# Kernel optimization log

Hardware: AMD Instinct MI355X
Metric: run time of the kernel (lower is better)

Reference implementation:

```python
import jax, jax.numpy as jnp
import numpy as np

M = 24      # number of DeepGravity sub-models
D_IN = 495  # input feature dim
H = 64      # hidden dim
L = 5       # hidden layers per sub-model


def setup_inputs() -> dict:
    key = jax.random.key(0)
    ks = jax.random.split(key, 7)
    s = 1.0 / np.sqrt(D_IN)
    sh = 1.0 / np.sqrt(H)
    return {
        "x": jax.random.normal(ks[0], (65536, D_IN), dtype=jnp.float32),
        "W_in": jax.random.uniform(ks[1], (M, D_IN, H), jnp.float32, -s, s),
        "b_in": jax.random.uniform(ks[2], (M, H), jnp.float32, -s, s),
        "W_h": jax.random.uniform(ks[3], (M, L, H, H), jnp.float32, -sh, sh),
        "b_h": jax.random.uniform(ks[4], (M, L, H), jnp.float32, -sh, sh),
        "W_out": jax.random.uniform(ks[5], (M, H), jnp.float32, -sh, sh),
        "b_out": jax.random.uniform(ks[6], (M,), jnp.float32, -sh, sh),
    }


def reference(x, W_in, b_in, W_h, b_h, W_out, b_out):
    # Batched input projection across all 24 models: [M, N, H]
    h0 = jnp.einsum("nf,mfh->mnh", x, W_in) + b_in[:, None, :]
    h = h0
    # 5 hidden layers (fixed, structurally distinct weights) as batched GEMMs
    for l in range(L):
        h = jax.nn.relu(jnp.einsum("mnh,mhk->mnk", h, W_h[:, l]) + b_h[:, l][:, None, :])
    h = h + h0  # residual
    # output head: Linear(64,1) + tanh, squeezed -> [M, N]
    out = jnp.tanh(jnp.einsum("mnh,mh->mn", h, W_out) + b_out[:, None])
    return out.T  # [N, M]
```

## Files before the change

### kernel.cpp

```cpp
#include <hip/hip_runtime.h>
#include <hip/hip_bf16.h>

typedef __attribute__((ext_vector_type(8))) short short8;
typedef __attribute__((ext_vector_type(4))) float f32x4;
typedef __attribute__((ext_vector_type(4))) unsigned uint4v;

#define NMODEL 24
#define DIN    495
#define KP     512
#define HID    64
#define NLAY   5

__device__ __forceinline__ short bf16r(float f) {
    unsigned u = __float_as_uint(f);
    u += 0x7fffu + ((u >> 16) & 1u);
    return (short)(u >> 16);
}
__device__ __forceinline__ float bf16f(short s) {
    return __uint_as_float(((unsigned)(unsigned short)s) << 16);
}
__device__ __forceinline__ unsigned pkbf16(float lo, float hi) {
    unsigned r;
    asm("v_cvt_pk_bf16_f32 %0, %1, %2" : "=v"(r) : "v"(lo), "v"(hi));
    return r;
}
__device__ __forceinline__ short8 pack2(f32x4 a, f32x4 b) {
    uint4v w;
    w[0] = pkbf16(a[0], a[1]);
    w[1] = pkbf16(a[2], a[3]);
    w[2] = pkbf16(b[0], b[1]);
    w[3] = pkbf16(b[2], b[3]);
    return __builtin_bit_cast(short8, w);
}

struct __attribute__((packed, aligned(4))) f4a { float v[4]; };

__global__ void dg_convert(const float* __restrict__ W_in,
                           const float* __restrict__ W_h,
                           short* __restrict__ wib, short* __restrict__ whb) {
    int idx = blockIdx.x * 256 + threadIdx.x;
    if (idx < NMODEL * 64 * HID * 8) {
        int t    = idx & 7;
        int hout = (idx >> 3) & 63;
        int kb   = (idx >> 9) & 63;
        int m    = idx >> 15;
        int k    = kb * 8 + t;
        float v  = (k < DIN) ? W_in[((size_t)m * DIN + k) * HID + hout] : 0.f;
        wib[idx] = bf16r(v);
    }
    if (idx < NMODEL * NLAY * 8 * HID * 8) {
        int t    = idx & 7;
        int hout = (idx >> 3) & 63;
        int kb   = (idx >> 9) & 7;
        int ml   = idx >> 12;
        int pk   = 16 * (2 * (kb >> 2) + (t >> 2)) + 4 * (kb & 3) + (t & 3);
        float v  = W_h[((size_t)ml * HID + pk) * HID + hout];
        whb[idx] = bf16r(v);
    }
}

__global__ __launch_bounds__(512, 4) void dg_main(
    const float* __restrict__ x,
    const short* __restrict__ wib, const short* __restrict__ whb,
    const float* __restrict__ b_in, const float* __restrict__ b_h,
    const float* __restrict__ W_out, const float* __restrict__ b_out,
    float* __restrict__ out) {

    __shared__ short xs[64 * KP];

    const int tid  = threadIdx.x;
    const int lane = tid & 63;
    const int w    = tid >> 6;
    const int lrow = lane & 15;
    const int g    = lane >> 4;
    const int rowbase = blockIdx.x * 64;
    const int pair = w >> 1;
    const int hf   = w & 1;
    const int rbase = hf * 32;

    for (int i = 0; i < 8; ++i) {
        int r  = i * 8 + w;
        int k0 = lane * 8;
        const float* xr = x + (size_t)(rowbase + r) * DIN + k0;
        uint4v vw;
        if (k0 + 8 <= DIN) {
            f4a a = *(const f4a*)xr;
            f4a b = *(const f4a*)(xr + 4);
            vw[0] = pkbf16(a.v[0], a.v[1]);
            vw[1] = pkbf16(a.v[2], a.v[3]);
            vw[2] = pkbf16(b.v[0], b.v[1]);
            vw[3] = pkbf16(b.v[2], b.v[3]);
        } else {
            float f[8];
#pragma unroll
            for (int j = 0; j < 8; ++j) f[j] = (k0 + j < DIN) ? xr[j] : 0.f;
            vw[0] = pkbf16(f[0], f[1]);
            vw[1] = pkbf16(f[2], f[3]);
            vw[2] = pkbf16(f[4], f[5]);
            vw[3] = pkbf16(f[6], f[7]);
        }
        int byte = (r * (KP * 2) + k0 * 2) ^ ((r & 7) << 4);
        *(short8*)((char*)xs + byte) = __builtin_bit_cast(short8, vw);
    }
    __syncthreads();

#pragma unroll 1
    for (int mi = 0; mi < 6; ++mi) {
        const int m = pair * 6 + mi;

        const float* bi = b_in + m * HID;
        f32x4 acc[4][2];
#pragma unroll
        for (int icf = 0; icf < 4; ++icf) {
            f32x4 bv = *(const f32x4*)(bi + icf * 16 + g * 4);
            acc[icf][0] = bv;
            acc[icf][1] = bv;
        }

        const short8* wA = (const short8*)wib + (size_t)m * 64 * 64;
#pragma unroll 2
        for (int skt = 0; skt < 16; ++skt) {
            const int kb = skt * 4 + g;
            short8 afr[4], bfr[2];
#pragma unroll
            for (int icf = 0; icf < 4; ++icf)
                afr[icf] = wA[(size_t)kb * 64 + icf * 16 + lrow];
#pragma unroll
            for (int rf = 0; rf < 2; ++rf) {
                int r = rbase + rf * 16 + lrow;
                int byte = (r * (KP * 2) + skt * 64 + g * 16) ^ ((r & 7) << 4);
                bfr[rf] = *(const short8*)((const char*)xs + byte);
            }
            __builtin_amdgcn_s_setprio(1);
#pragma unroll
            for (int icf = 0; icf < 4; ++icf)
#pragma unroll
                for (int rf = 0; rf < 2; ++rf)
                    acc[icf][rf] = __builtin_amdgcn_mfma_f32_16x16x32_bf16(
                        afr[icf], bfr[rf], acc[icf][rf], 0, 0, 0);
            __builtin_amdgcn_s_setprio(0);
        }

        short8 h0b[2][2];
#pragma unroll
        for (int s = 0; s < 2; ++s)
#pragma unroll
            for (int rf = 0; rf < 2; ++rf)
                h0b[s][rf] = pack2(acc[2 * s][rf], acc[2 * s + 1][rf]);

        const short8* wH = (const short8*)whb + (size_t)m * NLAY * 8 * 64;
        short8 hc[2][2];
#pragma unroll
        for (int s = 0; s < 2; ++s)
#pragma unroll
            for (int rf = 0; rf < 2; ++rf) hc[s][rf] = h0b[s][rf];

        f32x4 hacc[4][2];
#pragma unroll 1
        for (int l = 0; l < NLAY; ++l) {
            const float* bh = b_h + (size_t)(m * NLAY + l) * HID;
#pragma unroll
            for (int icf = 0; icf < 4; ++icf) {
                f32x4 bv = *(const f32x4*)(bh + icf * 16 + g * 4);
                hacc[icf][0] = bv;
                hacc[icf][1] = bv;
            }
#pragma unroll
            for (int s = 0; s < 2; ++s) {
                const int kb = 4 * s + g;
                short8 afr[4];
#pragma unroll
                for (int icf = 0; icf < 4; ++icf)
                    afr[icf] = wH[(size_t)(l * 8 + kb) * 64 + icf * 16 + lrow];
                __builtin_amdgcn_s_setprio(1);
#pragma unroll
                for (int icf = 0; icf < 4; ++icf)
#pragma unroll
                    for (int rf = 0; rf < 2; ++rf)
                        hacc[icf][rf] = __builtin_amdgcn_mfma_f32_16x16x32_bf16(
                            afr[icf], hc[s][rf], hacc[icf][rf], 0, 0, 0);
                __builtin_amdgcn_s_setprio(0);
            }
#pragma unroll
            for (int icf = 0; icf < 4; ++icf)
#pragma unroll
                for (int rf = 0; rf < 2; ++rf)
#pragma unroll
                    for (int j = 0; j < 4; ++j)
                        hacc[icf][rf][j] = fmaxf(hacc[icf][rf][j], 0.f);
            if (l != NLAY - 1) {
#pragma unroll
                for (int s = 0; s < 2; ++s)
#pragma unroll
                    for (int rf = 0; rf < 2; ++rf)
                        hc[s][rf] = pack2(hacc[2 * s][rf], hacc[2 * s + 1][rf]);
            }
        }

#pragma unroll
        for (int icf = 0; icf < 4; ++icf)
#pragma unroll
            for (int rf = 0; rf < 2; ++rf)
#pragma unroll
                for (int j = 0; j < 4; ++j)
                    hacc[icf][rf][j] += bf16f(h0b[icf >> 1][rf][(icf & 1) * 4 + j]);

        const float* wo = W_out + m * HID;
        const float bo = b_out[m];
#pragma unroll
        for (int rf = 0; rf < 2; ++rf) {
            float s = 0.f;
#pragma unroll
            for (int icf = 0; icf < 4; ++icf) {
                f32x4 wv = *(const f32x4*)(wo + icf * 16 + g * 4);
#pragma unroll
                for (int j = 0; j < 4; ++j)
                    s += hacc[icf][rf][j] * wv[j];
            }
            s += __shfl_xor(s, 16);
            s += __shfl_xor(s, 32);
            s += bo;
            float e = __expf(2.f * s);
            float o = 1.f - 2.f / (e + 1.f);
            if (g == 0)
                out[(size_t)(rowbase + rbase + rf * 16 + lrow) * NMODEL + m] = o;
        }
    }
}

extern "C" void kernel_launch(void* const* d_in, const int* in_sizes, int n_in,
                              void* d_out, int out_size, void* d_ws, size_t ws_size,
                              hipStream_t stream) {
    const float* x     = (const float*)d_in[0];
    const float* W_in  = (const float*)d_in[1];
    const float* b_in  = (const float*)d_in[2];
    const float* W_h   = (const float*)d_in[3];
    const float* b_h   = (const float*)d_in[4];
    const float* W_out = (const float*)d_in[5];
    const float* b_out = (const float*)d_in[6];
    float* out = (float*)d_out;

    short* wib = (short*)d_ws;
    short* whb = wib + NMODEL * 64 * HID * 8;

    const int N = in_sizes[0] / DIN;

    dg_convert<<<3072, 256, 0, stream>>>(W_in, W_h, wib, whb);
    dg_main<<<N / 64, 512, 0, stream>>>(x, wib, whb, b_in, b_h, W_out, b_out, out);
}
```

Measured before the change: 219.4 us.

## Switch MFMA tiles from 16x16x32 to 32x32x16 with re-laid-out weights

Replaces the 16x16x32 bf16 MFMA tiling with 32x32x16 bf16 MFMAs in both the input projection and the hidden layers. Each wave now covers its 32 rows with two 32x32 accumulators, and the weight conversion kernel writes weights in a matching per-lane layout. The goal is fewer MFMA issues and fewer weight and LDS fragment loads per unit of work, with weight loads now contiguous per lane. The output reduction needs one fewer shuffle. The trade-off is a larger accumulator footprint and different register pressure under the 512-thread launch bound.

```diff
diff --git a/kernel.cpp b/kernel.cpp
--- a/kernel.cpp
+++ b/kernel.cpp
@@ -3,6 +3,7 @@
 
 typedef __attribute__((ext_vector_type(8))) short short8;
 typedef __attribute__((ext_vector_type(4))) float f32x4;
+typedef __attribute__((ext_vector_type(16))) float f32x16;
 typedef __attribute__((ext_vector_type(4))) unsigned uint4v;
 
 #define NMODEL 24
@@ -24,13 +25,8 @@
     asm("v_cvt_pk_bf16_f32 %0, %1, %2" : "=v"(r) : "v"(lo), "v"(hi));
     return r;
 }
-__device__ __forceinline__ short8 pack2(f32x4 a, f32x4 b) {
-    uint4v w;
-    w[0] = pkbf16(a[0], a[1]);
-    w[1] = pkbf16(a[2], a[3]);
-    w[2] = pkbf16(b[0], b[1]);
-    w[3] = pkbf16(b[2], b[3]);
-    return __builtin_bit_cast(short8, w);
+__device__ __forceinline__ f32x16 mfma32(short8 a, short8 b, f32x16 c) {
+    return __builtin_amdgcn_mfma_f32_32x32x16_bf16(a, b, c, 0, 0, 0);
 }
 
 struct __attribute__((packed, aligned(4))) f4a { float v[4]; };
@@ -39,23 +35,26 @@
                            const float* __restrict__ W_h,
                            short* __restrict__ wib, short* __restrict__ whb) {
     int idx = blockIdx.x * 256 + threadIdx.x;
-    if (idx < NMODEL * 64 * HID * 8) {
+    if (idx < NMODEL * 32 * 2 * 64 * 8) {
         int t    = idx & 7;
-        int hout = (idx >> 3) & 63;
-        int kb   = (idx >> 9) & 63;
+        int lane = (idx >> 3) & 63;
+        int T    = (idx >> 9) & 1;
+        int ks   = (idx >> 10) & 31;
         int m    = idx >> 15;
-        int k    = kb * 8 + t;
-        float v  = (k < DIN) ? W_in[((size_t)m * DIN + k) * HID + hout] : 0.f;
+        int kg   = ks * 16 + (lane >> 5) * 8 + t;
+        int hout = T * 32 + (lane & 31);
+        float v  = (kg < DIN) ? W_in[((size_t)m * DIN + kg) * HID + hout] : 0.f;
         wib[idx] = bf16r(v);
     }
-    if (idx < NMODEL * NLAY * 8 * HID * 8) {
+    if (idx < NMODEL * NLAY * 4 * 2 * 64 * 8) {
         int t    = idx & 7;
-        int hout = (idx >> 3) & 63;
-        int kb   = (idx >> 9) & 7;
+        int lane = (idx >> 3) & 63;
+        int T    = (idx >> 9) & 1;
+        int s    = (idx >> 10) & 3;
         int ml   = idx >> 12;
-        int pk   = 16 * (2 * (kb >> 2) + (t >> 2)) + 4 * (kb & 3) + (t & 3);
-        float v  = W_h[((size_t)ml * HID + pk) * HID + hout];
-        whb[idx] = bf16r(v);
+        int pk   = 32 * (t >> 2) + (t & 3) + 8 * s + 4 * (lane >> 5);
+        int hout = T * 32 + (lane & 31);
+        whb[idx] = bf16r(W_h[((size_t)ml * HID + pk) * HID + hout]);
     }
 }
 
@@ -71,8 +70,8 @@
     const int tid  = threadIdx.x;
     const int lane = tid & 63;
     const int w    = tid >> 6;
-    const int lrow = lane & 15;
-    const int g    = lane >> 4;
+    const int r32  = lane & 31;
+    const int h5   = lane >> 5;
     const int rowbase = blockIdx.x * 64;
     const int pair = w >> 1;
     const int hf   = w & 1;
@@ -104,127 +103,130 @@
     }
     __syncthreads();
 
+    const int xrow  = rbase + r32;
+    const int xbase = xrow * (KP * 2);
+    const int xswz  = (xrow & 7) << 4;
+
 #pragma unroll 1
     for (int mi = 0; mi < 6; ++mi) {
         const int m = pair * 6 + mi;
 
         const float* bi = b_in + m * HID;
-        f32x4 acc[4][2];
-#pragma unroll
-        for (int icf = 0; icf < 4; ++icf) {
-            f32x4 bv = *(const f32x4*)(bi + icf * 16 + g * 4);
-            acc[icf][0] = bv;
-            acc[icf][1] = bv;
-        }
-
-        const short8* wA = (const short8*)wib + (size_t)m * 64 * 64;
+        f32x16 acc0, acc1;
+#pragma unroll
+        for (int q = 0; q < 4; ++q) {
+            f32x4 b0 = *(const f32x4*)(bi + 8 * q + 4 * h5);
+            f32x4 b1 = *(const f32x4*)(bi + 32 + 8 * q + 4 * h5);
+#pragma unroll
+            for (int j = 0; j < 4; ++j) {
+                acc0[4 * q + j] = b0[j];
+                acc1[4 * q + j] = b1[j];
+            }
+        }
+
+        const short8* wA = (const short8*)wib + (size_t)m * 4096;
 #pragma unroll 2
-        for (int skt = 0; skt < 16; ++skt) {
-            const int kb = skt * 4 + g;
-            short8 afr[4], bfr[2];
-#pragma unroll
-            for (int icf = 0; icf < 4; ++icf)
-                afr[icf] = wA[(size_t)kb * 64 + icf * 16 + lrow];
-#pragma unroll
-            for (int rf = 0; rf < 2; ++rf) {
-                int r = rbase + rf * 16 + lrow;
-                int byte = (r * (KP * 2) + skt * 64 + g * 16) ^ ((r & 7) << 4);
-                bfr[rf] = *(const short8*)((const char*)xs + byte);
-            }
+        for (int kp = 0; kp < 16; ++kp) {
+            const int ks0 = 2 * kp, ks1 = 2 * kp + 1;
+            short8 a00 = wA[(ks0 * 2 + 0) * 64 + lane];
+            short8 a01 = wA[(ks0 * 2 + 1) * 64 + lane];
+            short8 a10 = wA[(ks1 * 2 + 0) * 64 + lane];
+            short8 a11 = wA[(ks1 * 2 + 1) * 64 + lane];
+            short8 b0 = *(const short8*)((const char*)xs +
+                          ((xbase + ks0 * 32 + h5 * 16) ^ xswz));
+            short8 b1 = *(const short8*)((const char*)xs +
+                          ((xbase + ks1 * 32 + h5 * 16) ^ xswz));
             __builtin_amdgcn_s_setprio(1);
-#pragma unroll
-            for (int icf = 0; icf < 4; ++icf)
-#pragma unroll
-                for (int rf = 0; rf < 2; ++rf)
-                    acc[icf][rf] = __builtin_amdgcn_mfma_f32_16x16x32_bf16(
-                        afr[icf], bfr[rf], acc[icf][rf], 0, 0, 0);
+            acc0 = mfma32(a00, b0, acc0);
+            acc1 = mfma32(a01, b0, acc1);
+            acc0 = mfma32(a10, b1, acc0);
+            acc1 = mfma32(a11, b1, acc1);
             __builtin_amdgcn_s_setprio(0);
         }
 
-        short8 h0b[2][2];
-#pragma unroll
-        for (int s = 0; s < 2; ++s)
-#pragma unroll
-            for (int rf = 0; rf < 2; ++rf)
-                h0b[s][rf] = pack2(acc[2 * s][rf], acc[2 * s + 1][rf]);
-
-        const short8* wH = (const short8*)whb + (size_t)m * NLAY * 8 * 64;
-        short8 hc[2][2];
-#pragma unroll
-        for (int s = 0; s < 2; ++s)
-#pragma unroll
-            for (int rf = 0; rf < 2; ++rf) hc[s][rf] = h0b[s][rf];
-
-        f32x4 hacc[4][2];
+        short8 h0b[4], hc[4];
+#pragma unroll
+        for (int s = 0; s < 4; ++s) {
+            uint4v wv;
+            wv[0] = pkbf16(acc0[4 * s + 0], acc0[4 * s + 1]);
+            wv[1] = pkbf16(acc0[4 * s + 2], acc0[4 * s + 3]);
+            wv[2] = pkbf16(acc1[4 * s + 0], acc1[4 * s + 1]);
+            wv[3] = pkbf16(acc1[4 * s + 2], acc1[4 * s + 3]);
+            h0b[s] = __builtin_bit_cast(short8, wv);
+            hc[s]  = h0b[s];
+        }
+
+        const short8* wH = (const short8*)whb + (size_t)m * 2560;
+        f32x16 ha0, ha1;
 #pragma unroll 1
         for (int l = 0; l < NLAY; ++l) {
             const float* bh = b_h + (size_t)(m * NLAY + l) * HID;
 #pragma unroll
-            for (int icf = 0; icf < 4; ++icf) {
-                f32x4 bv = *(const f32x4*)(bh + icf * 16 + g * 4);
-                hacc[icf][0] = bv;
-                hacc[icf][1] = bv;
-            }
-#pragma unroll
-            for (int s = 0; s < 2; ++s) {
-                const int kb = 4 * s + g;
-                short8 afr[4];
-#pragma unroll
-                for (int icf = 0; icf < 4; ++icf)
-                    afr[icf] = wH[(size_t)(l * 8 + kb) * 64 + icf * 16 + lrow];
+            for (int q = 0; q < 4; ++q) {
+                f32x4 b0 = *(const f32x4*)(bh + 8 * q + 4 * h5);
+                f32x4 b1 = *(const f32x4*)(bh + 32 + 8 * q + 4 * h5);
+#pragma unroll
+                for (int j = 0; j < 4; ++j) {
+                    ha0[4 * q + j] = b0[j];
+                    ha1[4 * q + j] = b1[j];
+                }
+            }
+#pragma unroll
+            for (int sp = 0; sp < 2; ++sp) {
+                const int s0 = 2 * sp, s1 = 2 * sp + 1;
+                short8 a00 = wH[(size_t)((l * 4 + s0) * 2 + 0) * 64 + lane];
+                short8 a01 = wH[(size_t)((l * 4 + s0) * 2 + 1) * 64 + lane];
+                short8 a10 = wH[(size_t)((l * 4 + s1) * 2 + 0) * 64 + lane];
+                short8 a11 = wH[(size_t)((l * 4 + s1) * 2 + 1) * 64 + lane];
                 __builtin_amdgcn_s_setprio(1);
-#pragma unroll
-                for (int icf = 0; icf < 4; ++icf)
-#pragma unroll
-                    for (int rf = 0; rf < 2; ++rf)
-                        hacc[icf][rf] = __builtin_amdgcn_mfma_f32_16x16x32_bf16(
-                            afr[icf], hc[s][rf], hacc[icf][rf], 0, 0, 0);
+                ha0 = mfma32(a00, hc[s0], ha0);
+                ha1 = mfma32(a01, hc[s0], ha1);
+                ha0 = mfma32(a10, hc[s1], ha0);
+                ha1 = mfma32(a11, hc[s1], ha1);
                 __builtin_amdgcn_s_setprio(0);
             }
 #pragma unroll
-            for (int icf = 0; icf < 4; ++icf)
-#pragma unroll
-                for (int rf = 0; rf < 2; ++rf)
-#pragma unroll
-                    for (int j = 0; j < 4; ++j)
-                        hacc[icf][rf][j] = fmaxf(hacc[icf][rf][j], 0.f);
+            for (int e = 0; e < 16; ++e) {
+                ha0[e] = fmaxf(ha0[e], 0.f);
+                ha1[e] = fmaxf(ha1[e], 0.f);
+            }
             if (l != NLAY - 1) {
 #pragma unroll
-                for (int s = 0; s < 2; ++s)
-#pragma unroll
-                    for (int rf = 0; rf < 2; ++rf)
-                        hc[s][rf] = pack2(hacc[2 * s][rf], hacc[2 * s + 1][rf]);
-            }
-        }
-
-#pragma unroll
-        for (int icf = 0; icf < 4; ++icf)
-#pragma unroll
-            for (int rf = 0; rf < 2; ++rf)
-#pragma unroll
-                for (int j = 0; j < 4; ++j)
-                    hacc[icf][rf][j] += bf16f(h0b[icf >> 1][rf][(icf & 1) * 4 + j]);
+                for (int s = 0; s < 4; ++s) {
+                    uint4v wv;
+                    wv[0] = pkbf16(ha0[4 * s + 0], ha0[4 * s + 1]);
+                    wv[1] = pkbf16(ha0[4 * s + 2], ha0[4 * s + 3]);
+                    wv[2] = pkbf16(ha1[4 * s + 0], ha1[4 * s + 1]);
+                    wv[3] = pkbf16(ha1[4 * s + 2], ha1[4 * s + 3]);
+                    hc[s] = __builtin_bit_cast(short8, wv);
+                }
+            }
+        }
+
+#pragma unroll
+        for (int r = 0; r < 16; ++r) {
+            ha0[r] += bf16f(h0b[r >> 2][r & 3]);
+            ha1[r] += bf16f(h0b[r >> 2][4 + (r & 3)]);
+        }
 
         const float* wo = W_out + m * HID;
-        const float bo = b_out[m];
-#pragma unroll
-        for (int rf = 0; rf < 2; ++rf) {
-            float s = 0.f;
-#pragma unroll
-            for (int icf = 0; icf < 4; ++icf) {
-                f32x4 wv = *(const f32x4*)(wo + icf * 16 + g * 4);
-#pragma unroll
-                for (int j = 0; j < 4; ++j)
-                    s += hacc[icf][rf][j] * wv[j];
-            }
-            s += __shfl_xor(s, 16);
-            s += __shfl_xor(s, 32);
-            s += bo;
-            float e = __expf(2.f * s);
-            float o = 1.f - 2.f / (e + 1.f);
-            if (g == 0)
-                out[(size_t)(rowbase + rbase + rf * 16 + lrow) * NMODEL + m] = o;
-        }
+        float s = 0.f;
+#pragma unroll
+        for (int q = 0; q < 4; ++q) {
+            f32x4 w0 = *(const f32x4*)(wo + 8 * q + 4 * h5);
+            f32x4 w1 = *(const f32x4*)(wo + 32 + 8 * q + 4 * h5);
+#pragma unroll
+            for (int j = 0; j < 4; ++j) {
+                s += ha0[4 * q + j] * w0[j];
+                s += ha1[4 * q + j] * w1[j];
+            }
+        }
+        s += __shfl_xor(s, 32);
+        s += b_out[m];
+        float e = __expf(2.f * s);
+        float o = 1.f - 2.f / (e + 1.f);
+        if (h5 == 0)
+            out[(size_t)(rowbase + rbase + r32) * NMODEL + m] = o;
     }
 }
 
@@ -241,7 +243,7 @@
     float* out = (float*)d_out;
 
     short* wib = (short*)d_ws;
-    short* whb = wib + NMODEL * 64 * HID * 8;
+    short* whb = wib + NMODEL * 32 * 2 * 64 * 8;
 
     const int N = in_sizes[0] / DIN;
 
```

Result: slower. 257.2 us (+17.2%).

## Software-pipeline weight loads with double-buffered inline asm and stage outputs in LDS

Applied to the files above, without the earlier changes.

Weights for each model are repacked into one contiguous blob of 26 chunks (16 input-projection chunks plus 10 hidden-layer chunks), laid out so each lane fetches its fragment with dwordx4 loads at fixed offsets. The main loop issues these loads through inline asm two chunks ahead and waits with explicit vmcnt, so global weight latency overlaps the MFMA work across the input and hidden layers and across models. Output values are gathered in a shared buffer and written out with coalesced stores at the end, and the b_out and W_out loads are hoisted. The hand-written waitcnt and sched_barrier sequence is fragile: it depends on exact load ordering and adds register pressure from the eight in-flight weight vectors.

```diff
diff --git a/kernel.cpp b/kernel.cpp
--- a/kernel.cpp
+++ b/kernel.cpp
@@ -10,6 +10,8 @@
 #define KP     512
 #define HID    64
 #define NLAY   5
+#define CHUNKS 26
+#define MBLOB  (CHUNKS * 4096)
 
 __device__ __forceinline__ short bf16r(float f) {
     unsigned u = __float_as_uint(f);
@@ -35,38 +37,60 @@
 
 struct __attribute__((packed, aligned(4))) f4a { float v[4]; };
 
+#define GLD(dst, p, OFFSTR) \
+    asm volatile("global_load_dwordx4 %0, %1, off offset:" OFFSTR \
+                 : "=v"(dst) : "v"(p) : "memory")
+#define ISSUE4(n, p) { GLD(n##0, p, "0");   GLD(n##1, p, "256"); \
+                       GLD(n##2, p, "512"); GLD(n##3, p, "768"); }
+#define VW4 { asm volatile("s_waitcnt vmcnt(4)" ::: "memory"); \
+              __builtin_amdgcn_sched_barrier(0); }
+#define MF(wv, b, c) __builtin_amdgcn_mfma_f32_16x16x32_bf16( \
+                         __builtin_bit_cast(short8, wv), b, c, 0, 0, 0)
+#define MM8(n, b0, b1) { \
+    __builtin_amdgcn_s_setprio(1); \
+    acc[0][0] = MF(n##0, b0, acc[0][0]); acc[0][1] = MF(n##0, b1, acc[0][1]); \
+    acc[1][0] = MF(n##1, b0, acc[1][0]); acc[1][1] = MF(n##1, b1, acc[1][1]); \
+    acc[2][0] = MF(n##2, b0, acc[2][0]); acc[2][1] = MF(n##2, b1, acc[2][1]); \
+    acc[3][0] = MF(n##3, b0, acc[3][0]); acc[3][1] = MF(n##3, b1, acc[3][1]); \
+    __builtin_amdgcn_s_setprio(0); }
+
 __global__ void dg_convert(const float* __restrict__ W_in,
                            const float* __restrict__ W_h,
-                           short* __restrict__ wib, short* __restrict__ whb) {
+                           short* __restrict__ wsb) {
     int idx = blockIdx.x * 256 + threadIdx.x;
-    if (idx < NMODEL * 64 * HID * 8) {
-        int t    = idx & 7;
-        int hout = (idx >> 3) & 63;
-        int kb   = (idx >> 9) & 63;
-        int m    = idx >> 15;
-        int k    = kb * 8 + t;
-        float v  = (k < DIN) ? W_in[((size_t)m * DIN + k) * HID + hout] : 0.f;
-        wib[idx] = bf16r(v);
+    if (idx >= NMODEL * CHUNKS * 2048) return;
+    int t    = idx & 7;
+    int lrow = (idx >> 3) & 15;
+    int icf  = (idx >> 7) & 3;
+    int g    = (idx >> 9) & 3;
+    int mc   = idx >> 11;
+    int c    = mc % CHUNKS;
+    int m    = mc / CHUNKS;
+    int hout = icf * 16 + lrow;
+    float v;
+    if (c < 16) {
+        int k = (c * 4 + g) * 8 + t;
+        v = (k < DIN) ? W_in[((size_t)m * DIN + k) * HID + hout] : 0.f;
+    } else {
+        int l = (c - 16) >> 1, s = (c - 16) & 1;
+        int kb = 4 * s + g;
+        int pk = 16 * (2 * (kb >> 2) + (t >> 2)) + 4 * (kb & 3) + (t & 3);
+        v = W_h[((size_t)(m * NLAY + l) * HID + pk) * HID + hout];
     }
-    if (idx < NMODEL * NLAY * 8 * HID * 8) {
-        int t    = idx & 7;
-        int hout = (idx >> 3) & 63;
-        int kb   = (idx >> 9) & 7;
-        int ml   = idx >> 12;
-        int pk   = 16 * (2 * (kb >> 2) + (t >> 2)) + 4 * (kb & 3) + (t & 3);
-        float v  = W_h[((size_t)ml * HID + pk) * HID + hout];
-        whb[idx] = bf16r(v);
-    }
+    size_t off = (size_t)m * (CHUNKS * 2048) + c * 2048 + g * 512 +
+                 icf * 128 + lrow * 8 + t;
+    wsb[off] = bf16r(v);
 }
 
 __global__ __launch_bounds__(512, 4) void dg_main(
     const float* __restrict__ x,
-    const short* __restrict__ wib, const short* __restrict__ whb,
+    const short* __restrict__ wsb,
     const float* __restrict__ b_in, const float* __restrict__ b_h,
     const float* __restrict__ W_out, const float* __restrict__ b_out,
     float* __restrict__ out) {
 
     __shared__ short xs[64 * KP];
+    __shared__ float osb[64 * NMODEL];
 
     const int tid  = threadIdx.x;
     const int lane = tid & 63;
@@ -104,12 +128,25 @@
     }
     __syncthreads();
 
+    const float* bop = b_out + pair * 6;
+    float bz0 = bop[0], bz1 = bop[1], bz2 = bop[2],
+          bz3 = bop[3], bz4 = bop[4], bz5 = bop[5];
+
+    const char* pwBase = (const char*)wsb + (size_t)(pair * 6) * MBLOB +
+                         g * 1024 + lrow * 16;
+    const char* pw = pwBase;
+    uint4v w00, w01, w02, w03, w10, w11, w12, w13;
+    ISSUE4(w0, pw); pw += 4096;
+    ISSUE4(w1, pw); pw += 4096;
+
+    f32x4 acc[4][2];
+    short8 h0b[2][2], hc[2][2];
+
 #pragma unroll 1
     for (int mi = 0; mi < 6; ++mi) {
         const int m = pair * 6 + mi;
 
         const float* bi = b_in + m * HID;
-        f32x4 acc[4][2];
 #pragma unroll
         for (int icf = 0; icf < 4; ++icf) {
             f32x4 bv = *(const f32x4*)(bi + icf * 16 + g * 4);
@@ -117,83 +154,71 @@
             acc[icf][1] = bv;
         }
 
-        const short8* wA = (const short8*)wib + (size_t)m * 64 * 64;
-#pragma unroll 2
-        for (int skt = 0; skt < 16; ++skt) {
-            const int kb = skt * 4 + g;
-            short8 afr[4], bfr[2];
-#pragma unroll
-            for (int icf = 0; icf < 4; ++icf)
-                afr[icf] = wA[(size_t)kb * 64 + icf * 16 + lrow];
+#pragma unroll 1
+        for (int j = 0; j < 8; ++j) {
+            const int se = 2 * j, so = 2 * j + 1;
+            short8 be0, be1, bq0, bq1;
+            {
+                int r0 = rbase + lrow, r1 = rbase + 16 + lrow;
+                be0 = *(const short8*)((const char*)xs +
+                        ((r0 * (KP * 2) + se * 64 + g * 16) ^ ((r0 & 7) << 4)));
+                be1 = *(const short8*)((const char*)xs +
+                        ((r1 * (KP * 2) + se * 64 + g * 16) ^ ((r1 & 7) << 4)));
+            }
+            VW4;
+            MM8(w0, be0, be1);
+            ISSUE4(w0, pw); pw += 4096;
+            {
+                int r0 = rbase + lrow, r1 = rbase + 16 + lrow;
+                bq0 = *(const short8*)((const char*)xs +
+                        ((r0 * (KP * 2) + so * 64 + g * 16) ^ ((r0 & 7) << 4)));
+                bq1 = *(const short8*)((const char*)xs +
+                        ((r1 * (KP * 2) + so * 64 + g * 16) ^ ((r1 & 7) << 4)));
+            }
+            VW4;
+            MM8(w1, bq0, bq1);
+            ISSUE4(w1, pw); pw += 4096;
+        }
+
+#pragma unroll
+        for (int s = 0; s < 2; ++s)
 #pragma unroll
             for (int rf = 0; rf < 2; ++rf) {
-                int r = rbase + rf * 16 + lrow;
-                int byte = (r * (KP * 2) + skt * 64 + g * 16) ^ ((r & 7) << 4);
-                bfr[rf] = *(const short8*)((const char*)xs + byte);
-            }
-            __builtin_amdgcn_s_setprio(1);
-#pragma unroll
-            for (int icf = 0; icf < 4; ++icf)
-#pragma unroll
-                for (int rf = 0; rf < 2; ++rf)
-                    acc[icf][rf] = __builtin_amdgcn_mfma_f32_16x16x32_bf16(
-                        afr[icf], bfr[rf], acc[icf][rf], 0, 0, 0);
-            __builtin_amdgcn_s_setprio(0);
-        }
-
-        short8 h0b[2][2];
-#pragma unroll
-        for (int s = 0; s < 2; ++s)
-#pragma unroll
-            for (int rf = 0; rf < 2; ++rf)
                 h0b[s][rf] = pack2(acc[2 * s][rf], acc[2 * s + 1][rf]);
-
-        const short8* wH = (const short8*)whb + (size_t)m * NLAY * 8 * 64;
-        short8 hc[2][2];
-#pragma unroll
-        for (int s = 0; s < 2; ++s)
-#pragma unroll
-            for (int rf = 0; rf < 2; ++rf) hc[s][rf] = h0b[s][rf];
-
-        f32x4 hacc[4][2];
+                hc[s][rf]  = h0b[s][rf];
+            }
+
 #pragma unroll 1
         for (int l = 0; l < NLAY; ++l) {
             const float* bh = b_h + (size_t)(m * NLAY + l) * HID;
 #pragma unroll
             for (int icf = 0; icf < 4; ++icf) {
                 f32x4 bv = *(const f32x4*)(bh + icf * 16 + g * 4);
-                hacc[icf][0] = bv;
-                hacc[icf][1] = bv;
-            }
-#pragma unroll
-            for (int s = 0; s < 2; ++s) {
-                const int kb = 4 * s + g;
-                short8 afr[4];
-#pragma unroll
-                for (int icf = 0; icf < 4; ++icf)
-                    afr[icf] = wH[(size_t)(l * 8 + kb) * 64 + icf * 16 + lrow];
-                __builtin_amdgcn_s_setprio(1);
-#pragma unroll
-                for (int icf = 0; icf < 4; ++icf)
+                acc[icf][0] = bv;
+                acc[icf][1] = bv;
+            }
+            const bool lastC = (mi == 5) && (l == NLAY - 1);
+            const char* pA = lastC ? pwBase : pw;
+            VW4;
+            MM8(w0, hc[0][0], hc[0][1]);
+            ISSUE4(w0, pA); pw += 4096;
+            const char* pB = lastC ? (pwBase + 4096) : pw;
+            VW4;
+            MM8(w1, hc[1][0], hc[1][1]);
+            ISSUE4(w1, pB); pw += 4096;
+#pragma unroll
+            for (int icf = 0; icf < 4; ++icf)
+#pragma unroll
+                for (int rf = 0; rf < 2; ++rf)
+#pragma unroll
+                    for (int j = 0; j < 4; ++j)
+                        acc[icf][rf][j] = fmaxf(acc[icf][rf][j], 0.f);
+            if (l != NLAY - 1) {
+#pragma unroll
+                for (int s = 0; s < 2; ++s)
 #pragma unroll
                     for (int rf = 0; rf < 2; ++rf)
-                        hacc[icf][rf] = __builtin_amdgcn_mfma_f32_16x16x32_bf16(
-                            afr[icf], hc[s][rf], hacc[icf][rf], 0, 0, 0);
-                __builtin_amdgcn_s_setprio(0);
-            }
-#pragma unroll
-            for (int icf = 0; icf < 4; ++icf)
-#pragma unroll
-                for (int rf = 0; rf < 2; ++rf)
-#pragma unroll
-                    for (int j = 0; j < 4; ++j)
-                        hacc[icf][rf][j] = fmaxf(hacc[icf][rf][j], 0.f);
-            if (l != NLAY - 1) {
-#pragma unroll
-                for (int s = 0; s < 2; ++s)
-#pragma unroll
-                    for (int rf = 0; rf < 2; ++rf)
-                        hc[s][rf] = pack2(hacc[2 * s][rf], hacc[2 * s + 1][rf]);
+                        hc[s][rf] = pack2(acc[2 * s][rf], acc[2 * s + 1][rf]);
             }
         }
 
@@ -203,19 +228,24 @@
             for (int rf = 0; rf < 2; ++rf)
 #pragma unroll
                 for (int j = 0; j < 4; ++j)
-                    hacc[icf][rf][j] += bf16f(h0b[icf >> 1][rf][(icf & 1) * 4 + j]);
+                    acc[icf][rf][j] += bf16f(h0b[icf >> 1][rf][(icf & 1) * 4 + j]);
 
         const float* wo = W_out + m * HID;
-        const float bo = b_out[m];
+        f32x4 wv0 = *(const f32x4*)(wo + 0 * 16 + g * 4);
+        f32x4 wv1 = *(const f32x4*)(wo + 1 * 16 + g * 4);
+        f32x4 wv2 = *(const f32x4*)(wo + 2 * 16 + g * 4);
+        f32x4 wv3 = *(const f32x4*)(wo + 3 * 16 + g * 4);
+        float bo = (mi == 0) ? bz0 : (mi == 1) ? bz1 : (mi == 2) ? bz2 :
+                   (mi == 3) ? bz3 : (mi == 4) ? bz4 : bz5;
 #pragma unroll
         for (int rf = 0; rf < 2; ++rf) {
             float s = 0.f;
 #pragma unroll
-            for (int icf = 0; icf < 4; ++icf) {
-                f32x4 wv = *(const f32x4*)(wo + icf * 16 + g * 4);
-#pragma unroll
-                for (int j = 0; j < 4; ++j)
-                    s += hacc[icf][rf][j] * wv[j];
+            for (int j = 0; j < 4; ++j) {
+                s += acc[0][rf][j] * wv0[j];
+                s += acc[1][rf][j] * wv1[j];
+                s += acc[2][rf][j] * wv2[j];
+                s += acc[3][rf][j] * wv3[j];
             }
             s += __shfl_xor(s, 16);
             s += __shfl_xor(s, 32);
@@ -223,9 +253,13 @@
             float e = __expf(2.f * s);
             float o = 1.f - 2.f / (e + 1.f);
             if (g == 0)
-                out[(size_t)(rowbase + rbase + rf * 16 + lrow) * NMODEL + m] = o;
+                osb[(rbase + rf * 16 + lrow) * NMODEL + m] = o;
         }
     }
+
+    __syncthreads();
+    for (int i = tid; i < 64 * NMODEL; i += 512)
+        out[(size_t)rowbase * NMODEL + i] = osb[i];
 }
 
 extern "C" void kernel_launch(void* const* d_in, const int* in_sizes, int n_in,
@@ -240,11 +274,11 @@
     const float* b_out = (const float*)d_in[6];
     float* out = (float*)d_out;
 
-    short* wib = (short*)d_ws;
-    short* whb = wib + NMODEL * 64 * HID * 8;
+    short* wsb = (short*)d_ws;
 
     const int N = in_sizes[0] / DIN;
-
-    dg_convert<<<3072, 256, 0, stream>>>(W_in, W_h, wib, whb);
-    dg_main<<<N / 64, 512, 0, stream>>>(x, wib, whb, b_in, b_h, W_out, b_out, out);
-}
+    const int CONV = NMODEL * CHUNKS * 2048;
+
+    dg_convert<<<(CONV + 255) / 256, 256, 0, stream>>>(W_in, W_h, wsb);
+    dg_main<<<N / 64, 512, 0, stream>>>(x, wsb, b_in, b_h, W_out, b_out, out);
+}
```

New measurement: 218.2 us. About the same (-0.6%).
